# Performance work log

Measured on AMD Instinct MI355X. Metric: run time of the kernel, lower is better.

The kernel has to match this reference:

```python
import jax, jax.numpy as jnp
import numpy as np

EPS = 1e-8  # torch F.cosine_similarity default eps


def setup_inputs() -> dict:
    key = jax.random.key(0)
    k1, k2 = jax.random.split(key)
    xs_pad = jax.random.normal(k1, (8, 4096, 512), dtype=jnp.float32)
    spk_emb = jax.random.normal(k2, (8, 256, 512), dtype=jnp.float32)
    return {"xs_pad": xs_pad, "spk_emb": spk_emb}


def reference(xs_pad, spk_emb):
    # Faithful to F.cosine_similarity(x.unsqueeze(2), y.unsqueeze(1), dim=-1):
    #   dot(x, y) / (max(||x||, eps) * max(||y||, eps))
    # Implemented as L2-normalize then a batched GEMM -> (B, T, S), avoiding
    # the (B, T, S, D) broadcast intermediate.
    x_norm = jnp.maximum(jnp.linalg.norm(xs_pad, axis=-1, keepdims=True), EPS)
    y_norm = jnp.maximum(jnp.linalg.norm(spk_emb, axis=-1, keepdims=True), EPS)
    xn = xs_pad / x_norm          # (B, T, D)
    yn = spk_emb / y_norm         # (B, S, D)
    scores = jnp.einsum('btd,bsd->bts', xn, yn)  # (B, T, S)
    return scores
```

## Files before the change

kernel.cpp:

```cpp
#include <hip/hip_runtime.h>
#include <hip/hip_bf16.h>

#define BB 8
#define TT 4096
#define SS 256
#define DD 512

typedef __attribute__((ext_vector_type(8))) short short8;
typedef __attribute__((ext_vector_type(4))) float floatx4;
typedef __attribute__((ext_vector_type(4))) int intx4;

__device__ inline int pk2(float a, float b) {
  __hip_bfloat162 h = __float22bfloat162_rn(make_float2(a, b));
  int r;
  __builtin_memcpy(&r, &h, 4);
  return r;
}

__device__ inline short8 cvt8(float4 f0, float4 f1) {
  intx4 p;
  p[0] = pk2(f0.x, f0.y);
  p[1] = pk2(f0.z, f0.w);
  p[2] = pk2(f1.x, f1.y);
  p[3] = pk2(f1.z, f1.w);
  return __builtin_bit_cast(short8, p);
}

__global__ __launch_bounds__(256) void cos_fused_kernel(
    const float* __restrict__ xs, const float* __restrict__ spk,
    float* __restrict__ out) {
  __shared__ float sA[128 * 64];
  __shared__ float sB[128 * 64];
  __shared__ float scX[128];
  __shared__ float scY[128];

  const int tid = threadIdx.x;
  const int wave = tid >> 6;
  const int lane = tid & 63;
  const int tn = blockIdx.x;
  const int tm = blockIdx.y;
  const int b = blockIdx.z;

  const float* Abase = xs + ((size_t)b * TT + tm * 128) * DD;
  const float* Bbase = spk + ((size_t)b * SS + tn * 128) * DD;

  floatx4 acc[4][4];
#pragma unroll
  for (int i = 0; i < 4; i++)
#pragma unroll
    for (int j = 0; j < 4; j++) acc[i][j] = (floatx4){0.f, 0.f, 0.f, 0.f};
  floatx4 accG[4];
#pragma unroll
  for (int i = 0; i < 4; i++) accG[i] = (floatx4){0.f, 0.f, 0.f, 0.f};

  const int wm = wave >> 1;
  const int wn = wave & 1;
  const int quad = lane >> 4;
  const int l15 = lane & 15;
  const bool gramA = (wm == wn);

  int aoff[8];
#pragma unroll
  for (int j = 0; j < 8; j++) {
    int s = j * 256 + tid;
    int row = s >> 4;
    int blk = (s & 15) ^ (row & 15);
    aoff[j] = row * DD + blk * 4;
  }

  for (int kt = 0; kt < DD / 64; ++kt) {
#pragma unroll
    for (int j = 0; j < 8; j++) {
      const float* ga = Abase + aoff[j] + kt * 64;
      const float* gb = Bbase + aoff[j] + kt * 64;
      __builtin_amdgcn_global_load_lds(
          (const __attribute__((address_space(1))) unsigned int*)ga,
          (__attribute__((address_space(3))) unsigned int*)(sA +
              (j * 256 + wave * 64) * 4),
          16, 0, 0);
      __builtin_amdgcn_global_load_lds(
          (const __attribute__((address_space(1))) unsigned int*)gb,
          (__attribute__((address_space(3))) unsigned int*)(sB +
              (j * 256 + wave * 64) * 4),
          16, 0, 0);
    }
    __syncthreads();

#pragma unroll
    for (int ks = 0; ks < 2; ks++) {
      short8 af[4], bf[4];
      const int b0 = ks * 8 + quad * 2;
#pragma unroll
      for (int im = 0; im < 4; im++) {
        int row = wm * 64 + im * 16 + l15;
        int s0 = b0 ^ (row & 15);
        int s1 = (b0 + 1) ^ (row & 15);
        float4 f0 = *(const float4*)(sA + row * 64 + s0 * 4);
        float4 f1 = *(const float4*)(sA + row * 64 + s1 * 4);
        af[im] = cvt8(f0, f1);
      }
#pragma unroll
      for (int in = 0; in < 4; in++) {
        int row = wn * 64 + in * 16 + l15;
        int s0 = b0 ^ (row & 15);
        int s1 = (b0 + 1) ^ (row & 15);
        float4 f0 = *(const float4*)(sB + row * 64 + s0 * 4);
        float4 f1 = *(const float4*)(sB + row * 64 + s1 * 4);
        bf[in] = cvt8(f0, f1);
      }
#pragma unroll
      for (int im = 0; im < 4; im++)
#pragma unroll
        for (int in = 0; in < 4; in++)
          acc[im][in] = __builtin_amdgcn_mfma_f32_16x16x32_bf16(
              af[im], bf[in], acc[im][in], 0, 0, 0);
      if (gramA) {
#pragma unroll
        for (int im = 0; im < 4; im++)
          accG[im] = __builtin_amdgcn_mfma_f32_16x16x32_bf16(
              af[im], af[im], accG[im], 0, 0, 0);
      } else {
#pragma unroll
        for (int in = 0; in < 4; in++)
          accG[in] = __builtin_amdgcn_mfma_f32_16x16x32_bf16(
              bf[in], bf[in], accG[in], 0, 0, 0);
      }
    }
    __syncthreads();
  }

  if (quad == (l15 >> 2)) {
#pragma unroll
    for (int i = 0; i < 4; i++) {
      float inv = 1.0f / fmaxf(sqrtf(accG[i][l15 & 3]), 1e-8f);
      if (gramA)
        scX[wm * 64 + i * 16 + l15] = inv;
      else
        scY[wn * 64 + i * 16 + l15] = inv;
    }
  }
  __syncthreads();

  float* Obase = out + ((size_t)b * TT + tm * 128) * SS + tn * 128;
#pragma unroll
  for (int im = 0; im < 4; im++) {
#pragma unroll
    for (int in = 0; in < 4; in++) {
      int col = wn * 64 + in * 16 + l15;
      float yv = scY[col];
#pragma unroll
      for (int r = 0; r < 4; r++) {
        int row = wm * 64 + im * 16 + quad * 4 + r;
        Obase[row * SS + col] = acc[im][in][r] * scX[row] * yv;
      }
    }
  }
}

extern "C" void kernel_launch(void* const* d_in, const int* in_sizes, int n_in,
                              void* d_out, int out_size, void* d_ws,
                              size_t ws_size, hipStream_t stream) {
  const float* xs = (const float*)d_in[0];
  const float* spk = (const float*)d_in[1];
  float* out = (float*)d_out;

  hipLaunchKernelGGL(cos_fused_kernel, dim3(SS / 128, TT / 128, BB), dim3(256),
                     0, stream, xs, spk, out);
}
```

Before: 122.2 us.

## Load B operand fragments directly from global into registers, drop sB LDS tile

Removes the shared-memory staging buffer for the speaker-embedding tile. Each wave now loads its B fragments straight from global memory into registers and prefetches the second k-slice while the first is being used. This halves LDS traffic and LDS footprint, which may raise occupancy. In exchange, B data is no longer shared across waves, so global and L2 reads for B double, and the loads are exposed in registers with little latency hiding.

```diff
diff --git a/kernel.cpp b/kernel.cpp
--- a/kernel.cpp
+++ b/kernel.cpp
@@ -30,7 +30,6 @@
     const float* __restrict__ xs, const float* __restrict__ spk,
     float* __restrict__ out) {
   __shared__ float sA[128 * 64];
-  __shared__ float sB[128 * 64];
   __shared__ float scX[128];
   __shared__ float scY[128];
 
@@ -59,6 +58,11 @@
   const int l15 = lane & 15;
   const bool gramA = (wm == wn);
 
+  const float* bp[4];
+#pragma unroll
+  for (int in = 0; in < 4; in++)
+    bp[in] = Bbase + (size_t)(wn * 64 + in * 16 + l15) * DD + quad * 8;
+
   int aoff[8];
 #pragma unroll
   for (int j = 0; j < 8; j++) {
@@ -72,48 +76,50 @@
 #pragma unroll
     for (int j = 0; j < 8; j++) {
       const float* ga = Abase + aoff[j] + kt * 64;
-      const float* gb = Bbase + aoff[j] + kt * 64;
       __builtin_amdgcn_global_load_lds(
           (const __attribute__((address_space(1))) unsigned int*)ga,
           (__attribute__((address_space(3))) unsigned int*)(sA +
               (j * 256 + wave * 64) * 4),
           16, 0, 0);
-      __builtin_amdgcn_global_load_lds(
-          (const __attribute__((address_space(1))) unsigned int*)gb,
-          (__attribute__((address_space(3))) unsigned int*)(sB +
-              (j * 256 + wave * 64) * 4),
-          16, 0, 0);
+    }
+    float4 b0[4][2];
+#pragma unroll
+    for (int in = 0; in < 4; in++) {
+      const float* p = bp[in] + kt * 64;
+      b0[in][0] = *(const float4*)(p);
+      b0[in][1] = *(const float4*)(p + 4);
     }
     __syncthreads();
 
 #pragma unroll
     for (int ks = 0; ks < 2; ks++) {
-      short8 af[4], bf[4];
-      const int b0 = ks * 8 + quad * 2;
+      short8 af[4], bfr[4];
+      const int b0s = ks * 8 + quad * 2;
 #pragma unroll
       for (int im = 0; im < 4; im++) {
         int row = wm * 64 + im * 16 + l15;
-        int s0 = b0 ^ (row & 15);
-        int s1 = (b0 + 1) ^ (row & 15);
+        int s0 = b0s ^ (row & 15);
+        int s1 = (b0s + 1) ^ (row & 15);
         float4 f0 = *(const float4*)(sA + row * 64 + s0 * 4);
         float4 f1 = *(const float4*)(sA + row * 64 + s1 * 4);
         af[im] = cvt8(f0, f1);
       }
 #pragma unroll
-      for (int in = 0; in < 4; in++) {
-        int row = wn * 64 + in * 16 + l15;
-        int s0 = b0 ^ (row & 15);
-        int s1 = (b0 + 1) ^ (row & 15);
-        float4 f0 = *(const float4*)(sB + row * 64 + s0 * 4);
-        float4 f1 = *(const float4*)(sB + row * 64 + s1 * 4);
-        bf[in] = cvt8(f0, f1);
+      for (int in = 0; in < 4; in++) bfr[in] = cvt8(b0[in][0], b0[in][1]);
+      if (ks == 0) {
+#pragma unroll
+        for (int in = 0; in < 4; in++) {
+          const float* p = bp[in] + kt * 64 + 32;
+          b0[in][0] = *(const float4*)(p);
+          b0[in][1] = *(const float4*)(p + 4);
+        }
       }
 #pragma unroll
       for (int im = 0; im < 4; im++)
 #pragma unroll
         for (int in = 0; in < 4; in++)
           acc[im][in] = __builtin_amdgcn_mfma_f32_16x16x32_bf16(
-              af[im], bf[in], acc[im][in], 0, 0, 0);
+              af[im], bfr[in], acc[im][in], 0, 0, 0);
       if (gramA) {
 #pragma unroll
         for (int im = 0; im < 4; im++)
@@ -123,7 +129,7 @@
 #pragma unroll
         for (int in = 0; in < 4; in++)
           accG[in] = __builtin_amdgcn_mfma_f32_16x16x32_bf16(
-              bf[in], bf[in], accG[in], 0, 0, 0);
+              bfr[in], bfr[in], accG[in], 0, 0, 0);
       }
     }
     __syncthreads();
```

Measured after the change: 150.9 us. 23.5% more time.

## Double-buffer LDS tiles with K-step 32 and prefetch next tile

Applied to the files above, without the earlier changes.

The K tile shrinks from 64 to 32 and the shared-memory A and B tiles are double-buffered. While the MFMA work runs on the current buffer, the global-to-LDS loads for the next K step are already issued, and each iteration needs one barrier instead of two. The goal is to hide global load latency behind compute. The cost is twice as many loop iterations, a new XOR swizzle pattern, and a possible compiler-inserted vmcnt wait that could block the overlap.

```diff
diff --git a/kernel.cpp b/kernel.cpp
--- a/kernel.cpp
+++ b/kernel.cpp
@@ -29,8 +29,8 @@
 __global__ __launch_bounds__(256) void cos_fused_kernel(
     const float* __restrict__ xs, const float* __restrict__ spk,
     float* __restrict__ out) {
-  __shared__ float sA[128 * 64];
-  __shared__ float sB[128 * 64];
+  __shared__ float sA[2][128 * 32];
+  __shared__ float sB[2][128 * 32];
   __shared__ float scX[128];
   __shared__ float scY[128];
 
@@ -59,74 +59,92 @@
   const int l15 = lane & 15;
   const bool gramA = (wm == wn);
 
-  int aoff[8];
+  int aoff[4];
 #pragma unroll
-  for (int j = 0; j < 8; j++) {
+  for (int j = 0; j < 4; j++) {
     int s = j * 256 + tid;
-    int row = s >> 4;
-    int blk = (s & 15) ^ (row & 15);
+    int row = s >> 3;
+    int blk = (s & 7) ^ (row & 7);
     aoff[j] = row * DD + blk * 4;
   }
 
-  for (int kt = 0; kt < DD / 64; ++kt) {
 #pragma unroll
-    for (int j = 0; j < 8; j++) {
-      const float* ga = Abase + aoff[j] + kt * 64;
-      const float* gb = Bbase + aoff[j] + kt * 64;
-      __builtin_amdgcn_global_load_lds(
-          (const __attribute__((address_space(1))) unsigned int*)ga,
-          (__attribute__((address_space(3))) unsigned int*)(sA +
-              (j * 256 + wave * 64) * 4),
-          16, 0, 0);
-      __builtin_amdgcn_global_load_lds(
-          (const __attribute__((address_space(1))) unsigned int*)gb,
-          (__attribute__((address_space(3))) unsigned int*)(sB +
-              (j * 256 + wave * 64) * 4),
-          16, 0, 0);
-    }
+  for (int j = 0; j < 4; j++) {
+    __builtin_amdgcn_global_load_lds(
+        (const __attribute__((address_space(1))) unsigned int*)(Abase +
+            aoff[j]),
+        (__attribute__((address_space(3))) unsigned int*)(&sA[0][0] +
+            (j * 256 + wave * 64) * 4),
+        16, 0, 0);
+    __builtin_amdgcn_global_load_lds(
+        (const __attribute__((address_space(1))) unsigned int*)(Bbase +
+            aoff[j]),
+        (__attribute__((address_space(3))) unsigned int*)(&sB[0][0] +
+            (j * 256 + wave * 64) * 4),
+        16, 0, 0);
+  }
+
+  for (int kt = 0; kt < DD / 32; ++kt) {
     __syncthreads();
 
+    if (kt + 1 < DD / 32) {
+      const int nb = (kt + 1) & 1;
 #pragma unroll
-    for (int ks = 0; ks < 2; ks++) {
-      short8 af[4], bf[4];
-      const int b0 = ks * 8 + quad * 2;
+      for (int j = 0; j < 4; j++) {
+        __builtin_amdgcn_global_load_lds(
+            (const __attribute__((address_space(1))) unsigned int*)(Abase +
+                aoff[j] + (kt + 1) * 32),
+            (__attribute__((address_space(3))) unsigned int*)(&sA[nb][0] +
+                (j * 256 + wave * 64) * 4),
+            16, 0, 0);
+        __builtin_amdgcn_global_load_lds(
+            (const __attribute__((address_space(1))) unsigned int*)(Bbase +
+                aoff[j] + (kt + 1) * 32),
+            (__attribute__((address_space(3))) unsigned int*)(&sB[nb][0] +
+                (j * 256 + wave * 64) * 4),
+            16, 0, 0);
+      }
+    }
+
+    const float* cA = &sA[kt & 1][0];
+    const float* cB = &sB[kt & 1][0];
+    short8 af[4], bfr[4];
+    const int b0s = quad * 2;
 #pragma unroll
-      for (int im = 0; im < 4; im++) {
-        int row = wm * 64 + im * 16 + l15;
-        int s0 = b0 ^ (row & 15);
-        int s1 = (b0 + 1) ^ (row & 15);
-        float4 f0 = *(const float4*)(sA + row * 64 + s0 * 4);
-        float4 f1 = *(const float4*)(sA + row * 64 + s1 * 4);
-        af[im] = cvt8(f0, f1);
-      }
+    for (int im = 0; im < 4; im++) {
+      int row = wm * 64 + im * 16 + l15;
+      int s0 = b0s ^ (row & 7);
+      int s1 = (b0s + 1) ^ (row & 7);
+      float4 f0 = *(const float4*)(cA + row * 32 + s0 * 4);
+      float4 f1 = *(const float4*)(cA + row * 32 + s1 * 4);
+      af[im] = cvt8(f0, f1);
+    }
 #pragma unroll
-      for (int in = 0; in < 4; in++) {
-        int row = wn * 64 + in * 16 + l15;
-        int s0 = b0 ^ (row & 15);
-        int s1 = (b0 + 1) ^ (row & 15);
-        float4 f0 = *(const float4*)(sB + row * 64 + s0 * 4);
-        float4 f1 = *(const float4*)(sB + row * 64 + s1 * 4);
-        bf[in] = cvt8(f0, f1);
-      }
+    for (int in = 0; in < 4; in++) {
+      int row = wn * 64 + in * 16 + l15;
+      int s0 = b0s ^ (row & 7);
+      int s1 = (b0s + 1) ^ (row & 7);
+      float4 f0 = *(const float4*)(cB + row * 32 + s0 * 4);
+      float4 f1 = *(const float4*)(cB + row * 32 + s1 * 4);
+      bfr[in] = cvt8(f0, f1);
+    }
+#pragma unroll
+    for (int im = 0; im < 4; im++)
+#pragma unroll
+      for (int in = 0; in < 4; in++)
+        acc[im][in] = __builtin_amdgcn_mfma_f32_16x16x32_bf16(
+            af[im], bfr[in], acc[im][in], 0, 0, 0);
+    if (gramA) {
 #pragma unroll
       for (int im = 0; im < 4; im++)
+        accG[im] = __builtin_amdgcn_mfma_f32_16x16x32_bf16(
+            af[im], af[im], accG[im], 0, 0, 0);
+    } else {
 #pragma unroll
-        for (int in = 0; in < 4; in++)
-          acc[im][in] = __builtin_amdgcn_mfma_f32_16x16x32_bf16(
-              af[im], bf[in], acc[im][in], 0, 0, 0);
-      if (gramA) {
-#pragma unroll
-        for (int im = 0; im < 4; im++)
-          accG[im] = __builtin_amdgcn_mfma_f32_16x16x32_bf16(
-              af[im], af[im], accG[im], 0, 0, 0);
-      } else {
-#pragma unroll
-        for (int in = 0; in < 4; in++)
-          accG[in] = __builtin_amdgcn_mfma_f32_16x16x32_bf16(
-              bf[in], bf[in], accG[in], 0, 0, 0);
-      }
+      for (int in = 0; in < 4; in++)
+        accG[in] = __builtin_amdgcn_mfma_f32_16x16x32_bf16(
+            bfr[in], bfr[in], accG[in], 0, 0, 0);
     }
-    __syncthreads();
   }
 
   if (quad == (l15 >> 2)) {
```

Measured after the change: 124.9 us. 2.2% more time.
